# Optimization experiments

Hardware: AMD Instinct MI355X
Metric: run time of the kernel (lower is better)

## Reference

```python
import jax, jax.numpy as jnp
import numpy as np

N_EMBD = 1024
N_HEAD = 16
EPS = 1e-5

def layer_norm(x, g, b):
    mu = jnp.mean(x, axis=-1, keepdims=True)
    var = jnp.mean(jnp.square(x - mu), axis=-1, keepdims=True)
    return (x - mu) * jax.lax.rsqrt(var + EPS) * g + b

def setup_inputs() -> dict:
    key = jax.random.key(0)
    ks = jax.random.split(key, 12)
    C = N_EMBD
    s = lambda n: 1.0 / np.sqrt(n)
    return {
        "x": jax.random.normal(ks[0], (4, 2048, C), dtype=jnp.float32),
        "ln1_g": jnp.ones((C,), jnp.float32),
        "ln1_b": jnp.zeros((C,), jnp.float32),
        "attn_w": jax.random.normal(ks[1], (C, 3 * C), dtype=jnp.float32) * s(C),
        "attn_b": jnp.zeros((3 * C,), jnp.float32),
        "proj_w": jax.random.normal(ks[2], (C, C), dtype=jnp.float32) * s(C),
        "proj_b": jnp.zeros((C,), jnp.float32),
        "ln2_g": jnp.ones((C,), jnp.float32),
        "ln2_b": jnp.zeros((C,), jnp.float32),
        "fc1_w": jax.random.normal(ks[3], (C, 4 * C), dtype=jnp.float32) * s(C),
        "fc1_b": jnp.zeros((4 * C,), jnp.float32),
        "fc2_w": jax.random.normal(ks[4], (4 * C, C), dtype=jnp.float32) * s(4 * C),
        "fc2_b": jnp.zeros((C,), jnp.float32),
    }

def reference(x, ln1_g, ln1_b, attn_w, attn_b, proj_w, proj_b,
              ln2_g, ln2_b, fc1_w, fc1_b, fc2_w, fc2_b):
    B, T, C = x.shape
    H = N_HEAD
    D = C // H

    # --- self attention on ln1(x) ---
    h = layer_norm(x, ln1_g, ln1_b)
    qkv = h @ attn_w + attn_b                       # [B,T,3C]
    q, k, v = jnp.split(qkv, 3, axis=-1)
    q = q.reshape(B, T, H, D).transpose(0, 2, 1, 3)  # [B,H,T,D]
    k = k.reshape(B, T, H, D).transpose(0, 2, 1, 3)
    v = v.reshape(B, T, H, D).transpose(0, 2, 1, 3)
    att = jnp.einsum("bhqd,bhkd->bhqk", q, k) * (D ** -0.5)
    causal = jnp.tril(jnp.ones((T, T), dtype=bool))
    att = jnp.where(causal[None, None], att, -jnp.inf)
    att = jax.nn.softmax(att, axis=-1)
    y = jnp.einsum("bhqk,bhkd->bhqd", att, v)        # [B,H,T,D]
    y = y.transpose(0, 2, 1, 3).reshape(B, T, C)
    y = y @ proj_w + proj_b
    x = x + y

    # --- MLP on ln2(x) ---
    h = layer_norm(x, ln2_g, ln2_b)
    h = jax.nn.relu(h @ fc1_w + fc1_b)
    h = h @ fc2_w + fc2_b
    return x + h
```

## Files before the change

kernel.cpp:

```cpp
#include <hip/hip_runtime.h>
#include <cstdint>
#include <cstddef>

typedef __bf16 bf16x8 __attribute__((ext_vector_type(8)));
typedef float f32x4 __attribute__((ext_vector_type(4)));
typedef float f32x16 __attribute__((ext_vector_type(16)));
typedef unsigned short u16;
typedef unsigned uint2v __attribute__((ext_vector_type(2)));

namespace {
constexpr int Bb = 4, Tt = 2048, Cc = 1024, Hh = 16, Dd = 64;
constexpr int ROWS = Bb * Tt;
constexpr int C3 = 3 * Cc;
constexpr float LNEPS = 1e-5f;
constexpr float SCL2 = 0.18033688011112042f;
}

__device__ __forceinline__ u16 f2bf(float f) {
  union { float f; unsigned u; } v; v.f = f;
  return (u16)((v.u + 0x7fffu + ((v.u >> 16) & 1u)) >> 16);
}
__device__ __forceinline__ u16 bfn(float f) {
  union { __bf16 b; u16 u; } t; t.b = (__bf16)f; return t.u;
}
__device__ __forceinline__ unsigned pk2(float lo, float hi) {
  union { __bf16 b[2]; unsigned u; } t;
  t.b[0] = (__bf16)lo; t.b[1] = (__bf16)hi;
  return t.u;
}
__device__ __forceinline__ float exp2_hw(float x) {
  float r;
  asm("v_exp_f32 %0, %1" : "=v"(r) : "v"(x));
  return r;
}
__device__ __forceinline__ uint2v plswap(unsigned a, unsigned b) {
  return __builtin_amdgcn_permlane32_swap(a, b, false, false);
}
__device__ __forceinline__ float xhalf_max(float x) {
  union { float f; unsigned u; } c; c.f = x;
  uint2v r = plswap(c.u, c.u);
  union { unsigned u; float f; } a, b; a.u = r[0]; b.u = r[1];
  return fmaxf(a.f, b.f);
}
__device__ __forceinline__ float xhalf_sum(float x) {
  union { float f; unsigned u; } c; c.f = x;
  uint2v r = plswap(c.u, c.u);
  union { unsigned u; float f; } a, b; a.u = r[0]; b.u = r[1];
  return a.f + b.f;
}

typedef __attribute__((address_space(3))) unsigned lds_u32;
typedef __attribute__((address_space(1))) const unsigned glb_u32;
__device__ __forceinline__ void gload_lds16(const u16* g, u16* l) {
  __builtin_amdgcn_global_load_lds((glb_u32*)g, (lds_u32*)l, 16, 0, 0);
}

__global__ __launch_bounds__(256) void ln_kernel(
    const float* __restrict__ x, const float* __restrict__ g,
    const float* __restrict__ b, u16* __restrict__ out)
{
  const int row = blockIdx.x;
  const int tid = threadIdx.x;
  const float4 v = reinterpret_cast<const float4*>(x + (size_t)row * Cc)[tid];
  float s  = v.x + v.y + v.z + v.w;
  float ss = v.x * v.x + v.y * v.y + v.z * v.z + v.w * v.w;
#pragma unroll
  for (int off = 32; off; off >>= 1) {
    s  += __shfl_xor(s, off);
    ss += __shfl_xor(ss, off);
  }
  __shared__ float sa[4], sb[4];
  const int w = tid >> 6;
  if ((tid & 63) == 0) { sa[w] = s; sb[w] = ss; }
  __syncthreads();
  s  = sa[0] + sa[1] + sa[2] + sa[3];
  ss = sb[0] + sb[1] + sb[2] + sb[3];
  const float mu   = s * (1.0f / Cc);
  const float var  = ss * (1.0f / Cc) - mu * mu;
  const float rstd = rsqrtf(var + LNEPS);
  const float4 gv = reinterpret_cast<const float4*>(g)[tid];
  const float4 bv = reinterpret_cast<const float4*>(b)[tid];
  ushort4 o;
  o.x = f2bf((v.x - mu) * rstd * gv.x + bv.x);
  o.y = f2bf((v.y - mu) * rstd * gv.y + bv.y);
  o.z = f2bf((v.z - mu) * rstd * gv.z + bv.z);
  o.w = f2bf((v.w - mu) * rstd * gv.w + bv.w);
  reinterpret_cast<ushort4*>(out + (size_t)row * Cc)[tid] = o;
}

__global__ __launch_bounds__(256) void wcast_t(
    const float* __restrict__ w, u16* __restrict__ wt, int K, int N)
{
  __shared__ float tile[32][33];
  const int n0 = blockIdx.x * 32, k0 = blockIdx.y * 32;
  const int tx = threadIdx.x & 31, ty = threadIdx.x >> 5;
#pragma unroll
  for (int i = 0; i < 4; i++)
    tile[ty + i * 8][tx] = w[(size_t)(k0 + ty + i * 8) * N + n0 + tx];
  __syncthreads();
#pragma unroll
  for (int i = 0; i < 4; i++)
    wt[(size_t)(n0 + ty + i * 8) * K + k0 + tx] = f2bf(tile[tx][ty + i * 8]);
}

enum { EPI_BIAS_BF16 = 0, EPI_BIAS_RELU_BF16 = 1, EPI_BIAS_RES_F32 = 2 };

template <int EPI>
__global__ __launch_bounds__(256, 3) void gemm_bt2(
    const u16* __restrict__ A, const u16* __restrict__ Bt,
    const float* __restrict__ bias, const float* __restrict__ res,
    void* __restrict__ outp, int M, int N, int K)
{
  constexpr int BM = 128, BN = 128, BK = 64;
  __shared__ alignas(16) u16 As[BM][BK];
  __shared__ alignas(16) u16 Bs[BN][BK];
  const int tid  = threadIdx.x;
  const int lane = tid & 63;
  const int wv   = tid >> 6;
  const int wr   = wv >> 1, wc = wv & 1;
  const int lr   = lane & 15, lg = lane >> 4;

  const int xcd = (int)blockIdx.x & 7;
  const int j   = (int)blockIdx.x >> 3;
  const int nbn = N >> 7;
  const int bmpx = ((int)gridDim.x >> 3) / nbn;
  const int bm = (xcd * bmpx + j / nbn) << 7;
  const int bn = (j % nbn) << 7;

  f32x4 acc[4][4];
#pragma unroll
  for (int mi = 0; mi < 4; mi++)
#pragma unroll
    for (int nj = 0; nj < 4; nj++)
      acc[mi][nj] = (f32x4){0.f, 0.f, 0.f, 0.f};

  const int srow = tid >> 3;
  const int scol = ((tid & 7) ^ (srow & 7)) * 8;
  const u16* ga = &A [(size_t)(bm + srow) * K + scol];
  const u16* gb = &Bt[(size_t)(bn + srow) * K + scol];
  u16* as_dst = &As[0][0] + (size_t)tid * 8;
  u16* bs_dst = &Bs[0][0] + (size_t)tid * 8;

  for (int k0 = 0; k0 < K; k0 += BK) {
#pragma unroll
    for (int p = 0; p < 4; p++) {
      gload_lds16(ga + (size_t)p * 32 * K + k0, as_dst + p * 2048);
      gload_lds16(gb + (size_t)p * 32 * K + k0, bs_dst + p * 2048);
    }
    __syncthreads();
#pragma unroll
    for (int kk = 0; kk < BK; kk += 32) {
      const int cb = kk >> 3;
      const int csw = ((cb + lg) ^ (lr & 7)) * 8;
      bf16x8 af[4], bfr[4];
#pragma unroll
      for (int mi = 0; mi < 4; mi++)
        af[mi] = *reinterpret_cast<const bf16x8*>(&As[wr * 64 + mi * 16 + lr][0] + csw);
#pragma unroll
      for (int nj = 0; nj < 4; nj++)
        bfr[nj] = *reinterpret_cast<const bf16x8*>(&Bs[wc * 64 + nj * 16 + lr][0] + csw);
#pragma unroll
      for (int mi = 0; mi < 4; mi++)
#pragma unroll
        for (int nj = 0; nj < 4; nj++)
          acc[mi][nj] = __builtin_amdgcn_mfma_f32_16x16x32_bf16(af[mi], bfr[nj], acc[mi][nj], 0, 0, 0);
    }
    __syncthreads();
  }

#pragma unroll
  for (int mi = 0; mi < 4; mi++) {
#pragma unroll
    for (int nj = 0; nj < 4; nj++) {
      const int col = bn + wc * 64 + nj * 16 + lr;
      const float bv = bias[col];
#pragma unroll
      for (int r = 0; r < 4; r++) {
        const int row = bm + wr * 64 + mi * 16 + lg * 4 + r;
        float v = acc[mi][nj][r] + bv;
        if constexpr (EPI == EPI_BIAS_RELU_BF16) v = fmaxf(v, 0.0f);
        if constexpr (EPI == EPI_BIAS_RES_F32) {
          float* out = (float*)outp;
          out[(size_t)row * N + col] = v + res[(size_t)row * N + col];
        } else {
          ((u16*)outp)[(size_t)row * N + col] = f2bf(v);
        }
      }
    }
  }
}

__global__ __launch_bounds__(256) void build_vt(
    const u16* __restrict__ qkv, u16* __restrict__ vt)
{
  __shared__ u16 tile[64][80];
  const int t0 = blockIdx.x * 64;
  const int h  = blockIdx.y;
  const int b  = blockIdx.z;
  const int tid = threadIdx.x;
  const int rr = tid >> 3, cc = (tid & 7) * 8;
#pragma unroll
  for (int p = 0; p < 2; p++) {
    const int t = rr + p * 32;
    bf16x8 v = *reinterpret_cast<const bf16x8*>(
        &qkv[(size_t)(b * Tt + t0 + t) * C3 + 2 * Cc + h * Dd + cc]);
    *reinterpret_cast<bf16x8*>(&tile[t][cc]) = v;
  }
  __syncthreads();
#pragma unroll
  for (int p = 0; p < 2; p++) {
    const int d = rr + p * 32;
    union { u16 u[8]; int4 v; } o;
#pragma unroll
    for (int j = 0; j < 8; j++) o.u[j] = tile[cc + j][d];
    *reinterpret_cast<int4*>(&vt[(size_t)((b * Hh + h) * Dd + d) * Tt + t0 + cc]) = o.v;
  }
}

__global__ __launch_bounds__(512, 2) void flash_attn(
    const u16* __restrict__ qkv,
    const u16* __restrict__ vt,
    u16* __restrict__ y)
{
  const int tid = threadIdx.x, lane = tid & 63, wv = tid >> 6;
  const int l31 = lane & 31, hf = lane >> 5;

  const int bid = blockIdx.x;
  const int lid = (bid & 7) * 32 + (bid >> 3);
  const int bh = lid >> 2, pg = lid & 3;
  const int b = bh >> 4, h = bh & 15;
  const int sbase = pg * 4 + (wv & 3);
  const int s = (wv < 4) ? sbase : (31 - sbase);

  const u16* qbase = qkv + (size_t)b * Tt * C3 + h * Dd;
  const u16* kbase = qbase + Cc;
  const u16* vbase = vt + (size_t)bh * Dd * Tt;

  bool dmask[16];
#pragma unroll
  for (int r = 0; r < 16; r++)
    dmask[r] = ((r & 3) + 8 * (r >> 2) + 4 * hf) > l31;

  const int qa0 = s * 64;
  const int qb0 = qa0 + 32;
  const int ta = 2 * s;

  bf16x8 qfa[4], qfb[4];
#pragma unroll
  for (int kc = 0; kc < 4; kc++) {
    qfa[kc] = *reinterpret_cast<const bf16x8*>(
        &qbase[(size_t)(qa0 + l31) * C3 + kc * 16 + hf * 8]);
    qfb[kc] = *reinterpret_cast<const bf16x8*>(
        &qbase[(size_t)(qb0 + l31) * C3 + kc * 16 + hf * 8]);
  }

  f32x16 oa[2], ob[2];
#pragma unroll
  for (int i = 0; i < 16; i++) { oa[0][i] = 0.f; oa[1][i] = 0.f; ob[0][i] = 0.f; ob[1][i] = 0.f; }
  float mA = -INFINITY, lA = 0.0f, mB = -INFINITY, lB = 0.0f;

  const u16* kptr = &kbase[(size_t)l31 * C3 + hf * 8];
  const u16* vp0 = &vbase[(size_t)l31 * Tt + hf * 8];
  const u16* vp1 = vp0 + (size_t)32 * Tt;

  bf16x8 kf[4];
#pragma unroll
  for (int kc = 0; kc < 4; kc++)
    kf[kc] = *reinterpret_cast<const bf16x8*>(kptr + kc * 16);

  for (int kt = 0; kt <= ta; ++kt) {
    bf16x8 vf[2][2];
#pragma unroll
    for (int ch = 0; ch < 2; ch++) {
      vf[0][ch] = *reinterpret_cast<const bf16x8*>(vp0 + ch * 16);
      vf[1][ch] = *reinterpret_cast<const bf16x8*>(vp1 + ch * 16);
    }
    vp0 += 32; vp1 += 32;

    f32x16 sA, sB;
#pragma unroll
    for (int i = 0; i < 16; i++) { sA[i] = 0.f; sB[i] = 0.f; }
#pragma unroll
    for (int kc = 0; kc < 4; kc++) {
      sA = __builtin_amdgcn_mfma_f32_32x32x16_bf16(kf[kc], qfa[kc], sA, 0, 0, 0);
      sB = __builtin_amdgcn_mfma_f32_32x32x16_bf16(kf[kc], qfb[kc], sB, 0, 0, 0);
    }

    kptr += (size_t)32 * C3;
    bf16x8 kn[4];
#pragma unroll
    for (int kc = 0; kc < 4; kc++)
      kn[kc] = *reinterpret_cast<const bf16x8*>(kptr + kc * 16);

    const bool diagA = (kt == ta);

    float svA[16], svB[16];
#pragma unroll
    for (int r = 0; r < 16; r++) {
      svA[r] = sA[r];
      if (diagA && dmask[r]) svA[r] = -INFINITY;
      svB[r] = sB[r];
    }

    float mAa = fmaxf(fmaxf(svA[0], svA[1]), fmaxf(svA[2], svA[3]));
    float mAb = fmaxf(fmaxf(svA[4], svA[5]), fmaxf(svA[6], svA[7]));
    float mAc = fmaxf(fmaxf(svA[8], svA[9]), fmaxf(svA[10], svA[11]));
    float mAd = fmaxf(fmaxf(svA[12], svA[13]), fmaxf(svA[14], svA[15]));
    float m8A = fmaxf(fmaxf(mAa, mAb), fmaxf(mAc, mAd));
    float mBa = fmaxf(fmaxf(svB[0], svB[1]), fmaxf(svB[2], svB[3]));
    float mBb = fmaxf(fmaxf(svB[4], svB[5]), fmaxf(svB[6], svB[7]));
    float mBc = fmaxf(fmaxf(svB[8], svB[9]), fmaxf(svB[10], svB[11]));
    float mBd = fmaxf(fmaxf(svB[12], svB[13]), fmaxf(svB[14], svB[15]));
    float m8B = fmaxf(fmaxf(mBa, mBb), fmaxf(mBc, mBd));
    m8A = xhalf_max(m8A);
    m8B = xhalf_max(m8B);

    if (!__all(m8A - mA <= 64.0f)) {
      const float mnew  = fmaxf(mA, m8A);
      const float alpha = exp2_hw((mA - mnew) * SCL2);
      lA *= alpha;
#pragma unroll
      for (int i = 0; i < 16; i++) { oa[0][i] *= alpha; oa[1][i] *= alpha; }
      mA = mnew;
    }
    if (!__all(m8B - mB <= 64.0f)) {
      const float mnew  = fmaxf(mB, m8B);
      const float alpha = exp2_hw((mB - mnew) * SCL2);
      lB *= alpha;
#pragma unroll
      for (int i = 0; i < 16; i++) { ob[0][i] *= alpha; ob[1][i] *= alpha; }
      mB = mnew;
    }

    const float msA = mA * SCL2;
    const float msB = mB * SCL2;
    float pA[16], pB[16];
#pragma unroll
    for (int r = 0; r < 16; r++) {
      pA[r] = exp2_hw(fmaf(svA[r], SCL2, -msA));
      pB[r] = exp2_hw(fmaf(svB[r], SCL2, -msB));
    }
    {
      float a0 = ((pA[0] + pA[1]) + (pA[2] + pA[3])) + ((pA[4] + pA[5]) + (pA[6] + pA[7]));
      float a1 = ((pA[8] + pA[9]) + (pA[10] + pA[11])) + ((pA[12] + pA[13]) + (pA[14] + pA[15]));
      lA += a0 + a1;
      float b0 = ((pB[0] + pB[1]) + (pB[2] + pB[3])) + ((pB[4] + pB[5]) + (pB[6] + pB[7]));
      float b1 = ((pB[8] + pB[9]) + (pB[10] + pB[11])) + ((pB[12] + pB[13]) + (pB[14] + pB[15]));
      lB += b0 + b1;
    }

    unsigned pwA[2][4], pwB[2][4];
#pragma unroll
    for (int ch = 0; ch < 2; ch++) {
      const int bs = ch * 8;
      {
        unsigned w0 = pk2(pA[bs + 0], pA[bs + 1]);
        unsigned w1 = pk2(pA[bs + 2], pA[bs + 3]);
        unsigned w2 = pk2(pA[bs + 4], pA[bs + 5]);
        unsigned w3 = pk2(pA[bs + 6], pA[bs + 7]);
        uint2v r02 = plswap(w0, w2);
        uint2v r13 = plswap(w1, w3);
        pwA[ch][0] = r02[0]; pwA[ch][2] = r02[1];
        pwA[ch][1] = r13[0]; pwA[ch][3] = r13[1];
      }
      {
        unsigned w0 = pk2(pB[bs + 0], pB[bs + 1]);
        unsigned w1 = pk2(pB[bs + 2], pB[bs + 3]);
        unsigned w2 = pk2(pB[bs + 4], pB[bs + 5]);
        unsigned w3 = pk2(pB[bs + 6], pB[bs + 7]);
        uint2v r02 = plswap(w0, w2);
        uint2v r13 = plswap(w1, w3);
        pwB[ch][0] = r02[0]; pwB[ch][2] = r02[1];
        pwB[ch][1] = r13[0]; pwB[ch][3] = r13[1];
      }
    }

#pragma unroll
    for (int d0i = 0; d0i < 2; d0i++)
#pragma unroll
      for (int ch = 0; ch < 2; ch++) {
        union { unsigned w[4]; bf16x8 v; } pa, pb;
        pa.w[0] = pwA[ch][0]; pa.w[1] = pwA[ch][1];
        pa.w[2] = pwA[ch][2]; pa.w[3] = pwA[ch][3];
        pb.w[0] = pwB[ch][0]; pb.w[1] = pwB[ch][1];
        pb.w[2] = pwB[ch][2]; pb.w[3] = pwB[ch][3];
        oa[d0i] = __builtin_amdgcn_mfma_f32_32x32x16_bf16(vf[d0i][ch], pa.v, oa[d0i], 0, 0, 0);
        ob[d0i] = __builtin_amdgcn_mfma_f32_32x32x16_bf16(vf[d0i][ch], pb.v, ob[d0i], 0, 0, 0);
      }

#pragma unroll
    for (int kc = 0; kc < 4; kc++) kf[kc] = kn[kc];
  }

  {
    bf16x8 vf[2][2];
#pragma unroll
    for (int ch = 0; ch < 2; ch++) {
      vf[0][ch] = *reinterpret_cast<const bf16x8*>(vp0 + ch * 16);
      vf[1][ch] = *reinterpret_cast<const bf16x8*>(vp1 + ch * 16);
    }

    f32x16 sB;
#pragma unroll
    for (int i = 0; i < 16; i++) sB[i] = 0.f;
#pragma unroll
    for (int kc = 0; kc < 4; kc++)
      sB = __builtin_amdgcn_mfma_f32_32x32x16_bf16(kf[kc], qfb[kc], sB, 0, 0, 0);

    float svB[16];
#pragma unroll
    for (int r = 0; r < 16; r++) {
      svB[r] = sB[r];
      if (dmask[r]) svB[r] = -INFINITY;
    }
    float mBa = fmaxf(fmaxf(svB[0], svB[1]), fmaxf(svB[2], svB[3]));
    float mBb = fmaxf(fmaxf(svB[4], svB[5]), fmaxf(svB[6], svB[7]));
    float mBc = fmaxf(fmaxf(svB[8], svB[9]), fmaxf(svB[10], svB[11]));
    float mBd = fmaxf(fmaxf(svB[12], svB[13]), fmaxf(svB[14], svB[15]));
    float m8B = fmaxf(fmaxf(mBa, mBb), fmaxf(mBc, mBd));
    m8B = xhalf_max(m8B);

    if (!__all(m8B - mB <= 64.0f)) {
      const float mnew  = fmaxf(mB, m8B);
      const float alpha = exp2_hw((mB - mnew) * SCL2);
      lB *= alpha;
#pragma unroll
      for (int i = 0; i < 16; i++) { ob[0][i] *= alpha; ob[1][i] *= alpha; }
      mB = mnew;
    }
    const float msB = mB * SCL2;
    float pB[16];
#pragma unroll
    for (int r = 0; r < 16; r++)
      pB[r] = exp2_hw(fmaf(svB[r], SCL2, -msB));
    {
      float b0 = ((pB[0] + pB[1]) + (pB[2] + pB[3])) + ((pB[4] + pB[5]) + (pB[6] + pB[7]));
      float b1 = ((pB[8] + pB[9]) + (pB[10] + pB[11])) + ((pB[12] + pB[13]) + (pB[14] + pB[15]));
      lB += b0 + b1;
    }
    unsigned pwB[2][4];
#pragma unroll
    for (int ch = 0; ch < 2; ch++) {
      const int bs = ch * 8;
      unsigned w0 = pk2(pB[bs + 0], pB[bs + 1]);
      unsigned w1 = pk2(pB[bs + 2], pB[bs + 3]);
      unsigned w2 = pk2(pB[bs + 4], pB[bs + 5]);
      unsigned w3 = pk2(pB[bs + 6], pB[bs + 7]);
      uint2v r02 = plswap(w0, w2);
      uint2v r13 = plswap(w1, w3);
      pwB[ch][0] = r02[0]; pwB[ch][2] = r02[1];
      pwB[ch][1] = r13[0]; pwB[ch][3] = r13[1];
    }
#pragma unroll
    for (int d0i = 0; d0i < 2; d0i++)
#pragma unroll
      for (int ch = 0; ch < 2; ch++) {
        union { unsigned w[4]; bf16x8 v; } pb;
        pb.w[0] = pwB[ch][0]; pb.w[1] = pwB[ch][1];
        pb.w[2] = pwB[ch][2]; pb.w[3] = pwB[ch][3];
        ob[d0i] = __builtin_amdgcn_mfma_f32_32x32x16_bf16(vf[d0i][ch], pb.v, ob[d0i], 0, 0, 0);
      }
  }

  {
    const float lsA = xhalf_sum(lA);
    const float invA = 1.0f / lsA;
    u16* yrow = y + (size_t)(b * Tt + qa0 + l31) * Cc + h * Dd;
#pragma unroll
    for (int d0i = 0; d0i < 2; d0i++)
#pragma unroll
      for (int qd = 0; qd < 4; qd++) {
        ushort4 o;
        o.x = bfn(oa[d0i][qd * 4 + 0] * invA);
        o.y = bfn(oa[d0i][qd * 4 + 1] * invA);
        o.z = bfn(oa[d0i][qd * 4 + 2] * invA);
        o.w = bfn(oa[d0i][qd * 4 + 3] * invA);
        *reinterpret_cast<ushort4*>(&yrow[d0i * 32 + qd * 8 + hf * 4]) = o;
      }
  }
  {
    const float lsB = xhalf_sum(lB);
    const float invB = 1.0f / lsB;
    u16* yrow = y + (size_t)(b * Tt + qb0 + l31) * Cc + h * Dd;
#pragma unroll
    for (int d0i = 0; d0i < 2; d0i++)
#pragma unroll
      for (int qd = 0; qd < 4; qd++) {
        ushort4 o;
        o.x = bfn(ob[d0i][qd * 4 + 0] * invB);
        o.y = bfn(ob[d0i][qd * 4 + 1] * invB);
        o.z = bfn(ob[d0i][qd * 4 + 2] * invB);
        o.w = bfn(ob[d0i][qd * 4 + 3] * invB);
        *reinterpret_cast<ushort4*>(&yrow[d0i * 32 + qd * 8 + hf * 4]) = o;
      }
  }
}

extern "C" void kernel_launch(void* const* d_in, const int* in_sizes, int n_in,
                              void* d_out, int out_size, void* d_ws, size_t ws_size,
                              hipStream_t stream)
{
  const float* x      = (const float*)d_in[0];
  const float* ln1_g  = (const float*)d_in[1];
  const float* ln1_b  = (const float*)d_in[2];
  const float* attn_w = (const float*)d_in[3];
  const float* attn_b = (const float*)d_in[4];
  const float* proj_w = (const float*)d_in[5];
  const float* proj_b = (const float*)d_in[6];
  const float* ln2_g  = (const float*)d_in[7];
  const float* ln2_b  = (const float*)d_in[8];
  const float* fc1_w  = (const float*)d_in[9];
  const float* fc1_b  = (const float*)d_in[10];
  const float* fc2_w  = (const float*)d_in[11];
  const float* fc2_b  = (const float*)d_in[12];
  float* out = (float*)d_out;

  char* ws = (char*)d_ws;
  size_t o = 0;
  auto alloc = [&](size_t bytes) { char* p = ws + o; o += bytes; return p; };
  u16* wqkv_t  = (u16*)alloc((size_t)C3 * Cc * 2);
  u16* wproj_t = (u16*)alloc((size_t)Cc * Cc * 2);
  u16* wfc1_t  = (u16*)alloc((size_t)4096 * Cc * 2);
  u16* wfc2_t  = (u16*)alloc((size_t)Cc * 4096 * 2);
  u16* h_bf    = (u16*)alloc((size_t)ROWS * Cc * 2);
  u16* y_bf    = (u16*)alloc((size_t)ROWS * Cc * 2);
  u16* qkv_raw = (u16*)alloc((size_t)ROWS * C3 * 2);
  u16* vt      = (u16*)alloc((size_t)Bb * Hh * Dd * Tt * 2);
  u16* hh      = qkv_raw;

  wcast_t<<<dim3(C3 / 32, Cc / 32), 256, 0, stream>>>(attn_w, wqkv_t, Cc, C3);
  wcast_t<<<dim3(Cc / 32, Cc / 32), 256, 0, stream>>>(proj_w, wproj_t, Cc, Cc);
  wcast_t<<<dim3(4096 / 32, Cc / 32), 256, 0, stream>>>(fc1_w, wfc1_t, Cc, 4096);
  wcast_t<<<dim3(Cc / 32, 4096 / 32), 256, 0, stream>>>(fc2_w, wfc2_t, 4096, Cc);

  ln_kernel<<<ROWS, 256, 0, stream>>>(x, ln1_g, ln1_b, h_bf);
  gemm_bt2<EPI_BIAS_BF16><<<64 * (C3 / 128), 256, 0, stream>>>(
      h_bf, wqkv_t, attn_b, nullptr, qkv_raw, ROWS, C3, Cc);
  build_vt<<<dim3(Tt / 64, Hh, Bb), 256, 0, stream>>>(qkv_raw, vt);
  flash_attn<<<dim3(256), 512, 0, stream>>>(qkv_raw, vt, y_bf);
  gemm_bt2<EPI_BIAS_RES_F32><<<64 * (Cc / 128), 256, 0, stream>>>(
      y_bf, wproj_t, proj_b, x, out, ROWS, Cc, Cc);
  ln_kernel<<<ROWS, 256, 0, stream>>>(out, ln2_g, ln2_b, h_bf);
  gemm_bt2<EPI_BIAS_RELU_BF16><<<64 * (4096 / 128), 256, 0, stream>>>(
      h_bf, wfc1_t, fc1_b, nullptr, hh, ROWS, 4096, Cc);
  gemm_bt2<EPI_BIAS_RES_F32><<<64 * (Cc / 128), 256, 0, stream>>>(
      hh, wfc2_t, fc2_b, out, out, ROWS, Cc, 4096);
}
```

Baseline: 369.5 us.

## Fuse V-transpose into QKV GEMM epilogue, merge weight casts, wave-per-row layernorm

Drops the separate build_vt kernel by having the QKV GEMM epilogue write V transposed directly into the vt buffer. The four weight-cast launches are merged into one kernel with block-range dispatch. LayerNorm now uses one wave per row, which removes the shared-memory reduction and the block barrier. flash_attn launch bounds change from 2 to 1 blocks per CU, which may alter register allocation. Together these cut launch overhead and an extra read and write pass over V, at the cost of scattered 8-byte stores in the GEMM epilogue.

```diff
diff --git a/kernel.cpp b/kernel.cpp
--- a/kernel.cpp
+++ b/kernel.cpp
@@ -59,40 +59,56 @@
     const float* __restrict__ x, const float* __restrict__ g,
     const float* __restrict__ b, u16* __restrict__ out)
 {
-  const int row = blockIdx.x;
-  const int tid = threadIdx.x;
-  const float4 v = reinterpret_cast<const float4*>(x + (size_t)row * Cc)[tid];
-  float s  = v.x + v.y + v.z + v.w;
-  float ss = v.x * v.x + v.y * v.y + v.z * v.z + v.w * v.w;
-#pragma unroll
-  for (int off = 32; off; off >>= 1) {
+  const int row = blockIdx.x * 4 + (threadIdx.x >> 6);
+  const int l   = threadIdx.x & 63;
+  const float4* xr = reinterpret_cast<const float4*>(x + (size_t)row * Cc);
+  float4 v[4];
+  float s = 0.f, ss = 0.f;
+#pragma unroll
+  for (int i = 0; i < 4; i++) {
+    v[i] = xr[l + i * 64];
+    s  += v[i].x + v[i].y + v[i].z + v[i].w;
+    ss += v[i].x * v[i].x + v[i].y * v[i].y + v[i].z * v[i].z + v[i].w * v[i].w;
+  }
+#pragma unroll
+  for (int off = 1; off < 64; off <<= 1) {
     s  += __shfl_xor(s, off);
     ss += __shfl_xor(ss, off);
   }
-  __shared__ float sa[4], sb[4];
-  const int w = tid >> 6;
-  if ((tid & 63) == 0) { sa[w] = s; sb[w] = ss; }
-  __syncthreads();
-  s  = sa[0] + sa[1] + sa[2] + sa[3];
-  ss = sb[0] + sb[1] + sb[2] + sb[3];
   const float mu   = s * (1.0f / Cc);
   const float var  = ss * (1.0f / Cc) - mu * mu;
   const float rstd = rsqrtf(var + LNEPS);
-  const float4 gv = reinterpret_cast<const float4*>(g)[tid];
-  const float4 bv = reinterpret_cast<const float4*>(b)[tid];
-  ushort4 o;
-  o.x = f2bf((v.x - mu) * rstd * gv.x + bv.x);
-  o.y = f2bf((v.y - mu) * rstd * gv.y + bv.y);
-  o.z = f2bf((v.z - mu) * rstd * gv.z + bv.z);
-  o.w = f2bf((v.w - mu) * rstd * gv.w + bv.w);
-  reinterpret_cast<ushort4*>(out + (size_t)row * Cc)[tid] = o;
-}
-
-__global__ __launch_bounds__(256) void wcast_t(
-    const float* __restrict__ w, u16* __restrict__ wt, int K, int N)
+  const float4* gp = reinterpret_cast<const float4*>(g);
+  const float4* bp = reinterpret_cast<const float4*>(b);
+  ushort4* op = reinterpret_cast<ushort4*>(out + (size_t)row * Cc);
+#pragma unroll
+  for (int i = 0; i < 4; i++) {
+    const float4 gv = gp[l + i * 64];
+    const float4 bv = bp[l + i * 64];
+    ushort4 o;
+    o.x = f2bf((v[i].x - mu) * rstd * gv.x + bv.x);
+    o.y = f2bf((v[i].y - mu) * rstd * gv.y + bv.y);
+    o.z = f2bf((v[i].z - mu) * rstd * gv.z + bv.z);
+    o.w = f2bf((v[i].w - mu) * rstd * gv.w + bv.w);
+    op[l + i * 64] = o;
+  }
+}
+
+__global__ __launch_bounds__(256) void wcast_all(
+    const float* __restrict__ w0, u16* __restrict__ o0,
+    const float* __restrict__ w1, u16* __restrict__ o1,
+    const float* __restrict__ w2, u16* __restrict__ o2,
+    const float* __restrict__ w3, u16* __restrict__ o3)
 {
+  int bi = blockIdx.x;
+  const float* w; u16* wt; int K, N, nbx;
+  if (bi < 3072)      { w = w0; wt = o0; K = 1024; N = 3072; nbx = 96; }
+  else if (bi < 4096) { bi -= 3072; w = w1; wt = o1; K = 1024; N = 1024; nbx = 32; }
+  else if (bi < 8192) { bi -= 4096; w = w2; wt = o2; K = 1024; N = 4096; nbx = 128; }
+  else                { bi -= 8192; w = w3; wt = o3; K = 4096; N = 1024; nbx = 32; }
+  const int n0 = (bi % nbx) * 32, k0 = (bi / nbx) * 32;
+
   __shared__ float tile[32][33];
-  const int n0 = blockIdx.x * 32, k0 = blockIdx.y * 32;
   const int tx = threadIdx.x & 31, ty = threadIdx.x >> 5;
 #pragma unroll
   for (int i = 0; i < 4; i++)
@@ -105,11 +121,11 @@
 
 enum { EPI_BIAS_BF16 = 0, EPI_BIAS_RELU_BF16 = 1, EPI_BIAS_RES_F32 = 2 };
 
-template <int EPI>
+template <int EPI, bool FVT>
 __global__ __launch_bounds__(256, 3) void gemm_bt2(
     const u16* __restrict__ A, const u16* __restrict__ Bt,
     const float* __restrict__ bias, const float* __restrict__ res,
-    void* __restrict__ outp, int M, int N, int K)
+    void* __restrict__ outp, u16* __restrict__ vtout, int M, int N, int K)
 {
   constexpr int BM = 128, BN = 128, BK = 64;
   __shared__ alignas(16) u16 As[BM][BK];
@@ -174,50 +190,38 @@
     for (int nj = 0; nj < 4; nj++) {
       const int col = bn + wc * 64 + nj * 16 + lr;
       const float bv = bias[col];
+      const int row0 = bm + wr * 64 + mi * 16 + lg * 4;
+      u16 ov[4];
 #pragma unroll
       for (int r = 0; r < 4; r++) {
-        const int row = bm + wr * 64 + mi * 16 + lg * 4 + r;
+        const int row = row0 + r;
         float v = acc[mi][nj][r] + bv;
         if constexpr (EPI == EPI_BIAS_RELU_BF16) v = fmaxf(v, 0.0f);
         if constexpr (EPI == EPI_BIAS_RES_F32) {
           float* out = (float*)outp;
           out[(size_t)row * N + col] = v + res[(size_t)row * N + col];
         } else {
-          ((u16*)outp)[(size_t)row * N + col] = f2bf(v);
+          ov[r] = f2bf(v);
+          ((u16*)outp)[(size_t)row * N + col] = ov[r];
         }
       }
-    }
-  }
-}
-
-__global__ __launch_bounds__(256) void build_vt(
-    const u16* __restrict__ qkv, u16* __restrict__ vt)
-{
-  __shared__ u16 tile[64][80];
-  const int t0 = blockIdx.x * 64;
-  const int h  = blockIdx.y;
-  const int b  = blockIdx.z;
-  const int tid = threadIdx.x;
-  const int rr = tid >> 3, cc = (tid & 7) * 8;
-#pragma unroll
-  for (int p = 0; p < 2; p++) {
-    const int t = rr + p * 32;
-    bf16x8 v = *reinterpret_cast<const bf16x8*>(
-        &qkv[(size_t)(b * Tt + t0 + t) * C3 + 2 * Cc + h * Dd + cc]);
-    *reinterpret_cast<bf16x8*>(&tile[t][cc]) = v;
-  }
-  __syncthreads();
-#pragma unroll
-  for (int p = 0; p < 2; p++) {
-    const int d = rr + p * 32;
-    union { u16 u[8]; int4 v; } o;
-#pragma unroll
-    for (int j = 0; j < 8; j++) o.u[j] = tile[cc + j][d];
-    *reinterpret_cast<int4*>(&vt[(size_t)((b * Hh + h) * Dd + d) * Tt + t0 + cc]) = o.v;
-  }
-}
-
-__global__ __launch_bounds__(512, 2) void flash_attn(
+      if constexpr (FVT) {
+        if (col >= 2 * Cc) {
+          const int bq = row0 >> 11;
+          const int t0 = row0 & 2047;
+          const int hh2 = (col - 2 * Cc) >> 6;
+          const int dd2 = col & 63;
+          union { u16 u[4]; ushort4 v4; } pkv;
+          pkv.u[0] = ov[0]; pkv.u[1] = ov[1]; pkv.u[2] = ov[2]; pkv.u[3] = ov[3];
+          *reinterpret_cast<ushort4*>(
+              &vtout[((size_t)(bq * Hh + hh2) * Dd + dd2) * Tt + t0]) = pkv.v4;
+        }
+      }
+    }
+  }
+}
+
+__global__ __launch_bounds__(512, 1) void flash_attn(
     const u16* __restrict__ qkv,
     const u16* __restrict__ vt,
     u16* __restrict__ y)
@@ -528,21 +532,18 @@
   u16* vt      = (u16*)alloc((size_t)Bb * Hh * Dd * Tt * 2);
   u16* hh      = qkv_raw;
 
-  wcast_t<<<dim3(C3 / 32, Cc / 32), 256, 0, stream>>>(attn_w, wqkv_t, Cc, C3);
-  wcast_t<<<dim3(Cc / 32, Cc / 32), 256, 0, stream>>>(proj_w, wproj_t, Cc, Cc);
-  wcast_t<<<dim3(4096 / 32, Cc / 32), 256, 0, stream>>>(fc1_w, wfc1_t, Cc, 4096);
-  wcast_t<<<dim3(Cc / 32, 4096 / 32), 256, 0, stream>>>(fc2_w, wfc2_t, 4096, Cc);
-
-  ln_kernel<<<ROWS, 256, 0, stream>>>(x, ln1_g, ln1_b, h_bf);
-  gemm_bt2<EPI_BIAS_BF16><<<64 * (C3 / 128), 256, 0, stream>>>(
-      h_bf, wqkv_t, attn_b, nullptr, qkv_raw, ROWS, C3, Cc);
-  build_vt<<<dim3(Tt / 64, Hh, Bb), 256, 0, stream>>>(qkv_raw, vt);
+  wcast_all<<<12288, 256, 0, stream>>>(attn_w, wqkv_t, proj_w, wproj_t,
+                                       fc1_w, wfc1_t, fc2_w, wfc2_t);
+
+  ln_kernel<<<ROWS / 4, 256, 0, stream>>>(x, ln1_g, ln1_b, h_bf);
+  gemm_bt2<EPI_BIAS_BF16, true><<<64 * (C3 / 128), 256, 0, stream>>>(
+      h_bf, wqkv_t, attn_b, nullptr, qkv_raw, vt, ROWS, C3, Cc);
   flash_attn<<<dim3(256), 512, 0, stream>>>(qkv_raw, vt, y_bf);
-  gemm_bt2<EPI_BIAS_RES_F32><<<64 * (Cc / 128), 256, 0, stream>>>(
-      y_bf, wproj_t, proj_b, x, out, ROWS, Cc, Cc);
-  ln_kernel<<<ROWS, 256, 0, stream>>>(out, ln2_g, ln2_b, h_bf);
-  gemm_bt2<EPI_BIAS_RELU_BF16><<<64 * (4096 / 128), 256, 0, stream>>>(
-      h_bf, wfc1_t, fc1_b, nullptr, hh, ROWS, 4096, Cc);
-  gemm_bt2<EPI_BIAS_RES_F32><<<64 * (Cc / 128), 256, 0, stream>>>(
-      hh, wfc2_t, fc2_b, out, out, ROWS, Cc, 4096);
-}
+  gemm_bt2<EPI_BIAS_RES_F32, false><<<64 * (Cc / 128), 256, 0, stream>>>(
+      y_bf, wproj_t, proj_b, x, out, nullptr, ROWS, Cc, Cc);
+  ln_kernel<<<ROWS / 4, 256, 0, stream>>>(out, ln2_g, ln2_b, h_bf);
+  gemm_bt2<EPI_BIAS_RELU_BF16, false><<<64 * (4096 / 128), 256, 0, stream>>>(
+      h_bf, wfc1_t, fc1_b, nullptr, hh, nullptr, ROWS, 4096, Cc);
+  gemm_bt2<EPI_BIAS_RES_F32, false><<<64 * (Cc / 128), 256, 0, stream>>>(
+      hh, wfc2_t, fc2_b, out, out, nullptr, ROWS, Cc, 4096);
+}
```

After: 354.2 us. -4.2%, faster.
